# Kernel tuning notes

Hardware: AMD Instinct MI355X
Metric: run time of the kernel (lower is better)

Reference implementation:

```python
import jax, jax.numpy as jnp
import numpy as np

LN_EPS = 1e-5  # torch LayerNorm default
K_NN = 5       # top-5 nearest patterns (simple-surprise path)


def setup_inputs() -> dict:
    key = jax.random.key(0)
    ks = jax.random.split(key, 5)
    B, S, D, M = 8, 8192, 256, 50
    return {
        "hidden_states": jax.random.normal(ks[0], (B, S, D), dtype=jnp.float32),
        "memory": jax.random.normal(ks[1], (M, D), dtype=jnp.float32),
        "W1": jax.random.normal(ks[2], (D, 2 * D), dtype=jnp.float32) * (1.0 / np.sqrt(D)),
        "b1": jnp.zeros((2 * D,), dtype=jnp.float32),
        "W2": jax.random.normal(ks[3], (2 * D, D), dtype=jnp.float32) * (1.0 / np.sqrt(2 * D)),
        "b2": jnp.zeros((D,), dtype=jnp.float32),
        "ln_gamma": jnp.ones((D,), dtype=jnp.float32),
        "ln_beta": jnp.zeros((D,), dtype=jnp.float32),
    }


def reference(hidden_states, memory, W1, b1, W2, b2, ln_gamma, ln_beta):
    # Feature extractor: Linear -> ReLU -> (Dropout, eval=identity) -> Linear -> LayerNorm
    h = jax.nn.relu(jnp.einsum("bsd,de->bse", hidden_states, W1) + b1)
    f = jnp.einsum("bse,ed->bsd", h, W2) + b2
    mu = jnp.mean(f, axis=-1, keepdims=True)
    var = jnp.var(f, axis=-1, keepdims=True)
    feats = (f - mu) * jax.lax.rsqrt(var + LN_EPS) * ln_gamma + ln_beta  # [B,S,D]

    # Simple-surprise path, vectorized over all (b, s) tokens:
    # L2 distance of each token feature to every memory pattern.
    f_sq = jnp.sum(feats * feats, axis=-1)      # [B,S]
    m_sq = jnp.sum(memory * memory, axis=-1)    # [M]
    dots = jnp.einsum("bsd,md->bsm", feats, memory)  # [B,S,M]
    d2 = jnp.maximum(f_sq[..., None] + m_sq - 2.0 * dots, 0.0)
    dists = jnp.sqrt(d2)                        # [B,S,M]

    # k smallest distances -> mean -> sigmoid(avg - 1)
    neg_knn, _ = jax.lax.top_k(-dists, K_NN)    # [B,S,K]
    avg_dist = -jnp.mean(neg_knn, axis=-1)      # [B,S]
    surprise_scores = jax.nn.sigmoid(avg_dist - 1.0)
    return surprise_scores
```

## Files before the change

kernel.cpp:

```cpp
#include <hip/hip_runtime.h>
#include <math.h>

typedef __attribute__((ext_vector_type(8))) short bf16x8;
typedef __attribute__((ext_vector_type(4))) float f32x4;

static __device__ __forceinline__ unsigned short f2b(float x) {
  unsigned int u = __float_as_uint(x);
  u += 0x7FFFu + ((u >> 16) & 1u);
  return (unsigned short)(u >> 16);
}

__global__ void prep_weights(const float* __restrict__ W1,
                             const float* __restrict__ W2,
                             const float* __restrict__ mem,
                             unsigned short* __restrict__ W1T,
                             unsigned short* __restrict__ W2T,
                             unsigned short* __restrict__ memB) {
  int i = blockIdx.x * 256 + threadIdx.x;
  if (i < 131072) {
    int k = i >> 9, n = i & 511;
    W1T[n * 256 + k] = f2b(W1[i]);
  } else if (i < 262144) {
    int j = i - 131072;
    int k = j >> 8, n = j & 255;
    W2T[n * 512 + k] = f2b(W2[j]);
  } else if (i < 278528) {
    int j = i - 262144;
    int r = j >> 8;
    memB[j] = (r < 50) ? f2b(mem[j]) : (unsigned short)0;
  }
}

__global__ void prep_msq(const float* __restrict__ mem, float* __restrict__ msq) {
  int r = blockIdx.x;
  float s = 0.f;
  if (r < 50) {
    for (int c = threadIdx.x; c < 256; c += 64) {
      float v = mem[r * 256 + c];
      s += v * v;
    }
  }
  for (int m = 1; m < 64; m <<= 1) s += __shfl_xor(s, m, 64);
  if (threadIdx.x == 0) msq[r] = (r < 50) ? s : 1e30f;
}

#define XP 264
#define HP 136
#define DPitch 68

__global__ __launch_bounds__(256, 2) void fused_main(
    const float* __restrict__ X, const float* __restrict__ b1v,
    const float* __restrict__ b2v, const float* __restrict__ gammav,
    const float* __restrict__ betav, const unsigned short* __restrict__ W1T,
    const unsigned short* __restrict__ W2T,
    const unsigned short* __restrict__ memB, const float* __restrict__ msq,
    float* __restrict__ out) {
  __shared__ __align__(16) char smem[55040];
  unsigned short* Xs = (unsigned short*)smem;
  unsigned short* Hs = (unsigned short*)(smem + 33792);
  float* distS = (float*)(smem + 33792);
  float* red = (float*)(smem + 51200);
  float* psum   = red;
  float* psumsq = red + 256;
  float* fsqp   = red + 512;
  float* muS    = red + 768;
  float* rstdS  = red + 832;
  float* fsqS   = red + 896;

  const int tid = threadIdx.x;
  const int wid = tid >> 6;
  const int lane = tid & 63;
  const int l16 = lane & 15;
  const int quad = lane >> 4;

  const float4* X4 = (const float4*)(X + (size_t)blockIdx.x * 64 * 256);
#pragma unroll
  for (int j = 0; j < 16; ++j) {
    int idx = j * 256 + tid;
    float4 v = X4[idx];
    int row = idx >> 6, c4 = (idx & 63) << 2;
    unsigned int p0 = f2b(v.x) | ((unsigned int)f2b(v.y) << 16);
    unsigned int p1 = f2b(v.z) | ((unsigned int)f2b(v.w) << 16);
    *(uint2*)(&Xs[row * XP + c4]) = make_uint2(p0, p1);
  }

  f32x4 acc2[4][4];
#pragma unroll
  for (int mt = 0; mt < 4; ++mt) {
    const float4 bb = *(const float4*)(&b2v[wid * 64 + mt * 16 + quad * 4]);
#pragma unroll
    for (int nt = 0; nt < 4; ++nt) {
      acc2[mt][nt][0] = bb.x; acc2[mt][nt][1] = bb.y;
      acc2[mt][nt][2] = bb.z; acc2[mt][nt][3] = bb.w;
    }
  }

  __syncthreads();

  for (int cc = 0; cc < 4; ++cc) {
    int hbase = cc * 128 + wid * 32;
    f32x4 acc1[2][4];
#pragma unroll
    for (int mt = 0; mt < 2; ++mt) {
      const float4 bb = *(const float4*)(&b1v[hbase + mt * 16 + quad * 4]);
#pragma unroll
      for (int nt = 0; nt < 4; ++nt) {
        acc1[mt][nt][0] = bb.x; acc1[mt][nt][1] = bb.y;
        acc1[mt][nt][2] = bb.z; acc1[mt][nt][3] = bb.w;
      }
    }
#pragma unroll
    for (int kk = 0; kk < 8; ++kk) {
      int k0 = kk * 32 + quad * 8;
      bf16x8 a[2], b[4];
#pragma unroll
      for (int mt = 0; mt < 2; ++mt)
        a[mt] = *(const bf16x8*)(W1T + (hbase + mt * 16 + l16) * 256 + k0);
#pragma unroll
      for (int nt = 0; nt < 4; ++nt)
        b[nt] = *(const bf16x8*)(Xs + (nt * 16 + l16) * XP + k0);
#pragma unroll
      for (int mt = 0; mt < 2; ++mt)
#pragma unroll
        for (int nt = 0; nt < 4; ++nt)
          acc1[mt][nt] = __builtin_amdgcn_mfma_f32_16x16x32_bf16(
              a[mt], b[nt], acc1[mt][nt], 0, 0, 0);
    }
    __syncthreads();
#pragma unroll
    for (int mt = 0; mt < 2; ++mt) {
#pragma unroll
      for (int nt = 0; nt < 4; ++nt) {
        int token = nt * 16 + l16;
        int hloc = wid * 32 + mt * 16 + quad * 4;
        f32x4 v = acc1[mt][nt];
        unsigned int p0 = f2b(fmaxf(v[0], 0.f)) | ((unsigned int)f2b(fmaxf(v[1], 0.f)) << 16);
        unsigned int p1 = f2b(fmaxf(v[2], 0.f)) | ((unsigned int)f2b(fmaxf(v[3], 0.f)) << 16);
        *(uint2*)(&Hs[token * HP + hloc]) = make_uint2(p0, p1);
      }
    }
    __syncthreads();
#pragma unroll
    for (int k2 = 0; k2 < 4; ++k2) {
      int k0 = k2 * 32 + quad * 8;
      bf16x8 a[4], b[4];
#pragma unroll
      for (int mt = 0; mt < 4; ++mt)
        a[mt] = *(const bf16x8*)(W2T + (wid * 64 + mt * 16 + l16) * 512 + cc * 128 + k0);
#pragma unroll
      for (int nt = 0; nt < 4; ++nt)
        b[nt] = *(const bf16x8*)(Hs + (nt * 16 + l16) * HP + k0);
#pragma unroll
      for (int mt = 0; mt < 4; ++mt)
#pragma unroll
        for (int nt = 0; nt < 4; ++nt)
          acc2[mt][nt] = __builtin_amdgcn_mfma_f32_16x16x32_bf16(
              a[mt], b[nt], acc2[mt][nt], 0, 0, 0);
    }
  }

#pragma unroll
  for (int nt = 0; nt < 4; ++nt) {
    float s = 0.f, sq = 0.f;
#pragma unroll
    for (int mt = 0; mt < 4; ++mt)
#pragma unroll
      for (int r = 0; r < 4; ++r) {
        float v = acc2[mt][nt][r];
        s += v; sq += v * v;
      }
    s += __shfl_xor(s, 16, 64); sq += __shfl_xor(sq, 16, 64);
    s += __shfl_xor(s, 32, 64); sq += __shfl_xor(sq, 32, 64);
    if (quad == 0) {
      psum[wid * 64 + nt * 16 + l16] = s;
      psumsq[wid * 64 + nt * 16 + l16] = sq;
    }
  }
  __syncthreads();
  if (tid < 64) {
    float s = psum[tid] + psum[64 + tid] + psum[128 + tid] + psum[192 + tid];
    float sq = psumsq[tid] + psumsq[64 + tid] + psumsq[128 + tid] + psumsq[192 + tid];
    float mu = s * (1.f / 256.f);
    float var = sq * (1.f / 256.f) - mu * mu;
    muS[tid] = mu;
    rstdS[tid] = rsqrtf(var + 1e-5f);
  }
  __syncthreads();

  {
    float4 g[4], be[4];
#pragma unroll
    for (int mt = 0; mt < 4; ++mt) {
      g[mt]  = *(const float4*)(&gammav[wid * 64 + mt * 16 + quad * 4]);
      be[mt] = *(const float4*)(&betav[wid * 64 + mt * 16 + quad * 4]);
    }
#pragma unroll
    for (int nt = 0; nt < 4; ++nt) {
      int token = nt * 16 + l16;
      float mu = muS[token], rs = rstdS[token];
      float fs = 0.f;
#pragma unroll
      for (int mt = 0; mt < 4; ++mt) {
        float y0 = (acc2[mt][nt][0] - mu) * rs * g[mt].x + be[mt].x;
        float y1 = (acc2[mt][nt][1] - mu) * rs * g[mt].y + be[mt].y;
        float y2 = (acc2[mt][nt][2] - mu) * rs * g[mt].z + be[mt].z;
        float y3 = (acc2[mt][nt][3] - mu) * rs * g[mt].w + be[mt].w;
        fs += y0 * y0 + y1 * y1 + y2 * y2 + y3 * y3;
        unsigned int p0 = f2b(y0) | ((unsigned int)f2b(y1) << 16);
        unsigned int p1 = f2b(y2) | ((unsigned int)f2b(y3) << 16);
        *(uint2*)(&Xs[token * XP + wid * 64 + mt * 16 + quad * 4]) =
            make_uint2(p0, p1);
      }
      fs += __shfl_xor(fs, 16, 64);
      fs += __shfl_xor(fs, 32, 64);
      if (quad == 0) fsqp[wid * 64 + token] = fs;
    }
  }
  __syncthreads();
  if (tid < 64)
    fsqS[tid] = fsqp[tid] + fsqp[64 + tid] + fsqp[128 + tid] + fsqp[192 + tid];
  __syncthreads();

  f32x4 acc3[4];
#pragma unroll
  for (int nt = 0; nt < 4; ++nt) {
    acc3[nt][0] = 0.f; acc3[nt][1] = 0.f; acc3[nt][2] = 0.f; acc3[nt][3] = 0.f;
  }
#pragma unroll
  for (int kk = 0; kk < 8; ++kk) {
    int k0 = kk * 32 + quad * 8;
    bf16x8 a = *(const bf16x8*)(Xs + (wid * 16 + l16) * XP + k0);
#pragma unroll
    for (int nt = 0; nt < 4; ++nt) {
      bf16x8 b = *(const bf16x8*)(memB + (nt * 16 + l16) * 256 + k0);
      acc3[nt] = __builtin_amdgcn_mfma_f32_16x16x32_bf16(a, b, acc3[nt], 0, 0, 0);
    }
  }
  {
    float4 fsq4 = *(const float4*)(&fsqS[wid * 16 + quad * 4]);
#pragma unroll
    for (int nt = 0; nt < 4; ++nt) {
      int col = nt * 16 + l16;
      float mq = msq[col];
#pragma unroll
      for (int r = 0; r < 4; ++r) {
        float fv = (r == 0) ? fsq4.x : (r == 1) ? fsq4.y : (r == 2) ? fsq4.z : fsq4.w;
        float d2 = fv + mq - 2.f * acc3[nt][r];
        float d = sqrtf(fmaxf(d2, 0.f));
        int row = wid * 16 + quad * 4 + r;
        distS[row * DPitch + col] = d;
      }
    }
  }
  __syncthreads();

  if (tid < 64) {
    float b0 = 1e30f, b1 = 1e30f, b2 = 1e30f, b3 = 1e30f, b4 = 1e30f;
    const float* dr = &distS[tid * DPitch];
    for (int j = 0; j < 50; ++j) {
      float v = dr[j];
      b4 = fminf(b4, v);
      float t;
      if (b4 < b3) { t = b3; b3 = b4; b4 = t; }
      if (b3 < b2) { t = b2; b2 = b3; b3 = t; }
      if (b2 < b1) { t = b1; b1 = b2; b2 = t; }
      if (b1 < b0) { t = b0; b0 = b1; b1 = t; }
    }
    float avg = (b0 + b1 + b2 + b3 + b4) * 0.2f;
    float sarg = avg - 1.f;
    out[blockIdx.x * 64 + tid] = 1.f / (1.f + __expf(-sarg));
  }
}

extern "C" void kernel_launch(void* const* d_in, const int* in_sizes, int n_in,
                              void* d_out, int out_size, void* d_ws, size_t ws_size,
                              hipStream_t stream) {
  const float* X   = (const float*)d_in[0];
  const float* mem = (const float*)d_in[1];
  const float* W1  = (const float*)d_in[2];
  const float* b1  = (const float*)d_in[3];
  const float* W2  = (const float*)d_in[4];
  const float* b2  = (const float*)d_in[5];
  const float* g   = (const float*)d_in[6];
  const float* be  = (const float*)d_in[7];
  float* out = (float*)d_out;

  unsigned short* W1T  = (unsigned short*)d_ws;
  unsigned short* W2T  = W1T + 131072;
  unsigned short* memB = W2T + 131072;
  float* msq = (float*)(memB + 16384);

  prep_weights<<<1088, 256, 0, stream>>>(W1, W2, mem, W1T, W2T, memB);
  prep_msq<<<64, 64, 0, stream>>>(mem, msq);
  fused_main<<<1024, 256, 0, stream>>>(X, b1, b2, g, be, W1T, W2T, memB, msq, out);
}
```

Baseline: 189.2 us.

## Merge prep kernels with tiled transpose and raise main kernel occupancy

Replaces the two weight-prep kernels with a single kernel that transposes W1/W2 through shared-memory tiles (coalesced reads and writes) and computes memory squared norms alongside the bf16 conversion. The main kernel's launch bounds go from 2 to 3 blocks per CU, its LDS footprint shrinks slightly via a narrower distance pitch (65, also intended to avoid bank conflicts), and barriers are moved. The intent is to remove one launch and uncoalesced transposed stores, and to gain occupancy, at the cost of possible register spilling under the tighter launch bound.

Result: slower. 207.7 us (+9.8%).

```diff
diff --git a/kernel.cpp b/kernel.cpp
--- a/kernel.cpp
+++ b/kernel.cpp
@@ -3,6 +3,7 @@
 
 typedef __attribute__((ext_vector_type(8))) short bf16x8;
 typedef __attribute__((ext_vector_type(4))) float f32x4;
+typedef unsigned short ushort_t;
 
 static __device__ __forceinline__ unsigned short f2b(float x) {
   unsigned int u = __float_as_uint(x);
@@ -10,56 +11,82 @@
   return (unsigned short)(u >> 16);
 }
 
-__global__ void prep_weights(const float* __restrict__ W1,
-                             const float* __restrict__ W2,
-                             const float* __restrict__ mem,
-                             unsigned short* __restrict__ W1T,
-                             unsigned short* __restrict__ W2T,
-                             unsigned short* __restrict__ memB) {
-  int i = blockIdx.x * 256 + threadIdx.x;
-  if (i < 131072) {
-    int k = i >> 9, n = i & 511;
-    W1T[n * 256 + k] = f2b(W1[i]);
-  } else if (i < 262144) {
-    int j = i - 131072;
-    int k = j >> 8, n = j & 255;
-    W2T[n * 512 + k] = f2b(W2[j]);
-  } else if (i < 278528) {
-    int j = i - 262144;
-    int r = j >> 8;
-    memB[j] = (r < 50) ? f2b(mem[j]) : (unsigned short)0;
-  }
-}
-
-__global__ void prep_msq(const float* __restrict__ mem, float* __restrict__ msq) {
-  int r = blockIdx.x;
-  float s = 0.f;
-  if (r < 50) {
-    for (int c = threadIdx.x; c < 256; c += 64) {
-      float v = mem[r * 256 + c];
-      s += v * v;
-    }
-  }
-  for (int m = 1; m < 64; m <<= 1) s += __shfl_xor(s, m, 64);
-  if (threadIdx.x == 0) msq[r] = (r < 50) ? s : 1e30f;
+static __device__ __forceinline__ void transpose_tile(
+    const float* __restrict__ src, ushort_t* __restrict__ dst, int srcC,
+    int dstC, int r0, int c0, ushort_t (*T)[72], int t) {
+#pragma unroll
+  for (int j = 0; j < 4; ++j) {
+    int idx = j * 256 + t;
+    int lr = idx >> 4;
+    int lc = (idx & 15) << 2;
+    float4 v = *(const float4*)(&src[(size_t)(r0 + lr) * srcC + c0 + lc]);
+    T[lr][lc + 0] = f2b(v.x);
+    T[lr][lc + 1] = f2b(v.y);
+    T[lr][lc + 2] = f2b(v.z);
+    T[lr][lc + 3] = f2b(v.w);
+  }
+  __syncthreads();
+#pragma unroll
+  for (int j = 0; j < 2; ++j) {
+    int oidx = j * 256 + t;
+    int lc = oidx >> 3;
+    int rch = (oidx & 7) << 3;
+    ushort_t tmp[8];
+#pragma unroll
+    for (int k = 0; k < 8; ++k) tmp[k] = T[rch + k][lc];
+    *(uint4*)(&dst[(size_t)(c0 + lc) * dstC + r0 + rch]) = *(uint4*)tmp;
+  }
+}
+
+__global__ void prep(const float* __restrict__ W1, const float* __restrict__ W2,
+                     const float* __restrict__ mem, ushort_t* __restrict__ W1T,
+                     ushort_t* __restrict__ W2T, ushort_t* __restrict__ memB,
+                     float* __restrict__ msq) {
+  __shared__ ushort_t T[64][72];
+  int b = blockIdx.x;
+  int t = threadIdx.x;
+  if (b < 32) {
+    int tr = b >> 3, tc = b & 7;
+    transpose_tile(W1, W1T, 512, 256, tr * 64, tc * 64, T, t);
+  } else if (b < 64) {
+    int bb = b - 32;
+    int tr = bb >> 2, tc = bb & 3;
+    transpose_tile(W2, W2T, 256, 512, tr * 64, tc * 64, T, t);
+  } else {
+    for (int i = t; i < 16384; i += 256) {
+      int r = i >> 8;
+      memB[i] = (r < 50) ? f2b(mem[i]) : (ushort_t)0;
+    }
+    int r = t >> 2, seg = t & 3;
+    float s = 0.f;
+    if (r < 50) {
+#pragma unroll
+      for (int i = 0; i < 16; i += 4) {
+        float4 v = *(const float4*)(&mem[r * 256 + seg * 64 + i * 4]);
+        s += v.x * v.x + v.y * v.y + v.z * v.z + v.w * v.w;
+      }
+    }
+    s += __shfl_xor(s, 1, 64);
+    s += __shfl_xor(s, 2, 64);
+    if (seg == 0) msq[r] = (r < 50) ? s : 1e30f;
+  }
 }
 
 #define XP 264
 #define HP 136
-#define DPitch 68
-
-__global__ __launch_bounds__(256, 2) void fused_main(
+#define DPitch 65
+
+__global__ __launch_bounds__(256, 3) void fused_main(
     const float* __restrict__ X, const float* __restrict__ b1v,
     const float* __restrict__ b2v, const float* __restrict__ gammav,
-    const float* __restrict__ betav, const unsigned short* __restrict__ W1T,
-    const unsigned short* __restrict__ W2T,
-    const unsigned short* __restrict__ memB, const float* __restrict__ msq,
-    float* __restrict__ out) {
-  __shared__ __align__(16) char smem[55040];
-  unsigned short* Xs = (unsigned short*)smem;
-  unsigned short* Hs = (unsigned short*)(smem + 33792);
+    const float* __restrict__ betav, const ushort_t* __restrict__ W1T,
+    const ushort_t* __restrict__ W2T, const ushort_t* __restrict__ memB,
+    const float* __restrict__ msq, float* __restrict__ out) {
+  __shared__ __align__(16) char smem[54272];
+  ushort_t* Xs = (ushort_t*)smem;
+  ushort_t* Hs = (ushort_t*)(smem + 33792);
   float* distS = (float*)(smem + 33792);
-  float* red = (float*)(smem + 51200);
+  float* red = (float*)(smem + 50432);
   float* psum   = red;
   float* psumsq = red + 256;
   float* fsqp   = red + 512;
@@ -158,6 +185,7 @@
               a[mt], b[nt], acc2[mt][nt], 0, 0, 0);
     }
   }
+  __syncthreads();
 
 #pragma unroll
   for (int nt = 0; nt < 4; ++nt) {
@@ -217,9 +245,9 @@
     }
   }
   __syncthreads();
+
   if (tid < 64)
     fsqS[tid] = fsqp[tid] + fsqp[64 + tid] + fsqp[128 + tid] + fsqp[192 + tid];
-  __syncthreads();
 
   f32x4 acc3[4];
 #pragma unroll
@@ -236,6 +264,7 @@
       acc3[nt] = __builtin_amdgcn_mfma_f32_16x16x32_bf16(a, b, acc3[nt], 0, 0, 0);
     }
   }
+  __syncthreads();
   {
     float4 fsq4 = *(const float4*)(&fsqS[wid * 16 + quad * 4]);
 #pragma unroll
@@ -285,12 +314,11 @@
   const float* be  = (const float*)d_in[7];
   float* out = (float*)d_out;
 
-  unsigned short* W1T  = (unsigned short*)d_ws;
-  unsigned short* W2T  = W1T + 131072;
-  unsigned short* memB = W2T + 131072;
+  ushort_t* W1T  = (ushort_t*)d_ws;
+  ushort_t* W2T  = W1T + 131072;
+  ushort_t* memB = W2T + 131072;
   float* msq = (float*)(memB + 16384);
 
-  prep_weights<<<1088, 256, 0, stream>>>(W1, W2, mem, W1T, W2T, memB);
-  prep_msq<<<64, 64, 0, stream>>>(mem, msq);
+  prep<<<65, 256, 0, stream>>>(W1, W2, mem, W1T, W2T, memB, msq);
   fused_main<<<1024, 256, 0, stream>>>(X, b1, b2, g, be, W1T, W2T, memB, msq, out);
 }
```
